# Performance work log

Hardware: AMD Instinct MI355X
Metric: run time of the kernel (lower is better)

The kernel has to match this reference:

```python
import jax, jax.numpy as jnp
import numpy as np

BITS = 16          # number of histogram bins == number of spiking time steps
B, IN_DIM, HID = 16384, 784, 128


def setup_inputs() -> dict:
    key = jax.random.key(0)
    ks = jax.random.split(key, 9)
    dims = [(HID, IN_DIM), (HID, HID), (HID, HID), (IN_DIM, HID)]
    inp = {"features": jax.random.uniform(ks[0], (B, IN_DIM), jnp.float32)}
    for i, (o, d) in enumerate(dims):
        inp["W%d" % i] = jax.random.normal(ks[1 + i], (o, d), jnp.float32) * 0.05
        inp["b%d" % i] = jax.random.normal(ks[5 + i], (o,), jnp.float32) * 0.05
    # np.histogram_bin_edges(bins=16) -> 17 uniformly spaced edges per layer
    in_max = [1.0, 4.0, 4.0, 4.0]
    out_max = [4.0, 4.0, 4.0, 4.0]
    for i in range(4):
        inp["in_bins%d" % i] = jnp.linspace(0.0, in_max[i], BITS + 1, dtype=jnp.float32)
        inp["out_bins%d" % i] = jnp.linspace(0.0, out_max[i], BITS + 1, dtype=jnp.float32)
    return inp


def _spike(t):
    # output[output>1]=1; output[output<1]=0  (==1 stays 1)  -> (t >= 1)
    # totals[output==1] -= 1
    s = (t >= 1.0).astype(t.dtype)
    return s, t - s


def _forward(features, Ws, bs, in_bins, out_bins):
    h_in = [e[1] - e[0] for e in in_bins]    # uniform spike heights
    h_out = [e[1] - e[0] for e in out_bins]
    # set_up_weights: weight *= h_in; weight /= h_out (bias likewise)
    Weff = [Ws[l] * (h_in[l] / h_out[l]) for l in range(4)]
    beff = [bs[l] * (h_in[l] / h_out[l]) for l in range(4)]
    n = features.shape[0]
    # discretize: np.digitize(x, in_bins) - 1, then / 16.0 (non-differentiable)
    act = (jnp.digitize(jax.lax.stop_gradient(features), in_bins[0]) - 1).astype(features.dtype) / BITS
    t_in = jnp.zeros_like(features)                               # input-layer membrane
    totals = tuple(jnp.broadcast_to(beff[l], (n,) + beff[l].shape) for l in range(4))  # reset_totals: totals = bias
    out_acc = jnp.zeros((n, Weff[3].shape[0]), features.dtype)

    def step(carry, _):
        t_in, t0, t1, t2, t3, out = carry
        s_in, t_in = _spike(t_in + act)
        # process_layer: totals += sum(weight * spikes, axis=1) == spikes @ W.T
        s0, t0 = _spike(t0 + s_in @ Weff[0].T)
        s1, t1 = _spike(t1 + s0 @ Weff[1].T)
        s2, t2 = _spike(t2 + s1 @ Weff[2].T)
        s3, t3 = _spike(t3 + s2 @ Weff[3].T)
        return (t_in, t0, t1, t2, t3, out + s3), None

    carry, _ = jax.lax.scan(step, (t_in,) + totals + (out_acc,), None, length=BITS)
    out_spikes = carry[-1]
    # decoder_output_layer.reconstruct: spikes * (out_bins[1] - out_bins[0])
    return out_spikes * h_out[3]


def reference(features, W0, W1, W2, W3, b0, b1, b2, b3,
              in_bins0, in_bins1, in_bins2, in_bins3,
              out_bins0, out_bins1, out_bins2, out_bins3):
    return _forward(features,
                    [W0, W1, W2, W3], [b0, b1, b2, b3],
                    [in_bins0, in_bins1, in_bins2, in_bins3],
                    [out_bins0, out_bins1, out_bins2, out_bins3])
```

## Files before the change

### kernel.cpp

```cpp
#include <hip/hip_runtime.h>

#define IN_DIM 784
#define HID 128
#define NSTEP 16
#define BATCH 16384

constexpr int W0T_OFF = 0;
constexpr int W1T_OFF = W0T_OFF + IN_DIM*HID;
constexpr int W2T_OFF = W1T_OFF + HID*HID;
constexpr int W3T_OFF = W2T_OFF + HID*HID;
constexpr int B0_OFF  = W3T_OFF + HID*IN_DIM;
constexpr int B1_OFF  = B0_OFF + HID;
constexpr int B2_OFF  = B1_OFF + HID;
constexpr int B3_OFF  = B2_OFF + HID;
constexpr int WS_FLOATS = B3_OFF + IN_DIM;

__global__ __launch_bounds__(256) void prep_kernel(
    const float* __restrict__ W0, const float* __restrict__ b0,
    const float* __restrict__ W1, const float* __restrict__ b1,
    const float* __restrict__ W2, const float* __restrict__ b2,
    const float* __restrict__ W3, const float* __restrict__ b3,
    const float* __restrict__ ib0, const float* __restrict__ ob0,
    const float* __restrict__ ib1, const float* __restrict__ ob1,
    const float* __restrict__ ib2, const float* __restrict__ ob2,
    const float* __restrict__ ib3, const float* __restrict__ ob3,
    float* __restrict__ ws)
{
    int idx = blockIdx.x * 256 + threadIdx.x;
    if (idx >= WS_FLOATS) return;
    float r0 = (ib0[1] - ib0[0]) / (ob0[1] - ob0[0]);
    float r1 = (ib1[1] - ib1[0]) / (ob1[1] - ob1[0]);
    float r2 = (ib2[1] - ib2[0]) / (ob2[1] - ob2[0]);
    float r3 = (ib3[1] - ib3[0]) / (ob3[1] - ob3[0]);
    if (idx < W1T_OFF) {
        int t = idx;            int k = t >> 7, j = t & 127;
        ws[idx] = W0[j * IN_DIM + k] * r0;
    } else if (idx < W2T_OFF) {
        int t = idx - W1T_OFF;  int k = t >> 7, j = t & 127;
        ws[idx] = W1[j * HID + k] * r1;
    } else if (idx < W3T_OFF) {
        int t = idx - W2T_OFF;  int k = t >> 7, j = t & 127;
        ws[idx] = W2[j * HID + k] * r2;
    } else if (idx < B0_OFF) {
        int t = idx - W3T_OFF;  int k = t / IN_DIM, o = t % IN_DIM;
        ws[idx] = W3[o * HID + k] * r3;
    } else if (idx < B1_OFF) ws[idx] = b0[idx - B0_OFF] * r0;
    else if (idx < B2_OFF)   ws[idx] = b1[idx - B1_OFF] * r1;
    else if (idx < B3_OFF)   ws[idx] = b2[idx - B2_OFF] * r2;
    else                     ws[idx] = b3[idx - B3_OFF] * r3;
}

__global__ __launch_bounds__(256) void snn_main(
    const float* __restrict__ feat,
    const float* __restrict__ ws,
    const float* __restrict__ ib0,
    const float* __restrict__ ob3,
    float* __restrict__ out)
{
    const int lane = threadIdx.x & 63;
    const int sample = blockIdx.x * 4 + (threadIdx.x >> 6);

    const float* W0t = ws + W0T_OFF;
    const float* W1t = ws + W1T_OFF;
    const float* W2t = ws + W2T_OFF;
    const float* W3t = ws + W3T_OFF;

    float edge[16];
#pragma unroll
    for (int e = 0; e < 16; ++e) edge[e] = ib0[e + 1];

    int m[13];
    {
        const float* frow = feat + (size_t)sample * IN_DIM;
#pragma unroll
        for (int r = 0; r < 13; ++r) {
            int idx = r * 64 + lane;
            int mm = 0;
            if (idx < IN_DIM) {
                float x = frow[idx];
#pragma unroll
                for (int e = 0; e < 16; ++e) mm += (x >= edge[e]) ? 1 : 0;
            }
            m[r] = mm;
        }
    }

    float2 C[16];
#pragma unroll
    for (int mv = 1; mv <= 16; ++mv) {
        float2 ca = make_float2(0.f, 0.f), cb = make_float2(0.f, 0.f);
#pragma unroll
        for (int r = 0; r < 13; ++r) {
            unsigned long long mk = __ballot(m[r] == mv);
            while (mk) {
                int b0 = __builtin_ctzll(mk); mk &= mk - 1;
                float2 w0 = ((const float2*)(W0t + (unsigned)((r << 6) + b0) * HID))[lane];
                if (mk) {
                    int b1 = __builtin_ctzll(mk); mk &= mk - 1;
                    float2 w1 = ((const float2*)(W0t + (unsigned)((r << 6) + b1) * HID))[lane];
                    if (mk) {
                        int b2 = __builtin_ctzll(mk); mk &= mk - 1;
                        float2 w2 = ((const float2*)(W0t + (unsigned)((r << 6) + b2) * HID))[lane];
                        if (mk) {
                            int b3i = __builtin_ctzll(mk); mk &= mk - 1;
                            float2 w3 = ((const float2*)(W0t + (unsigned)((r << 6) + b3i) * HID))[lane];
                            cb.x += w3.x; cb.y += w3.y;
                        }
                        ca.x += w2.x; ca.y += w2.y;
                    }
                    cb.x += w1.x; cb.y += w1.y;
                }
                ca.x += w0.x; ca.y += w0.y;
            }
        }
        C[mv - 1] = make_float2(ca.x + cb.x, ca.y + cb.y);
    }

    float2 t0 = ((const float2*)(ws + B0_OFF))[lane];
    float2 t1 = ((const float2*)(ws + B1_OFF))[lane];
    float2 t2 = ((const float2*)(ws + B2_OFF))[lane];
    float4 t3[4], cnt[4];
    {
        const float4* b3v = (const float4*)(ws + B3_OFF);
#pragma unroll
        for (int r = 0; r < 3; ++r) t3[r] = b3v[r * 64 + lane];
        t3[3] = make_float4(0.f, 0.f, 0.f, 0.f);
        if (lane < 4) t3[3] = b3v[192 + lane];
#pragma unroll
        for (int r = 0; r < 4; ++r) cnt[r] = make_float4(0.f, 0.f, 0.f, 0.f);
    }

    for (int s = 1; s <= NSTEP; ++s) {
#pragma unroll
        for (int mv = 1; mv <= 16; ++mv) {
            if (((s * mv) & 15) < mv) { t0.x += C[mv - 1].x; t0.y += C[mv - 1].y; }
        }
        {
            bool px = (t0.x >= 1.0f), py = (t0.y >= 1.0f);
            unsigned long long mx = __ballot(px);
            unsigned long long my = __ballot(py);
            if (px) t0.x -= 1.0f;
            if (py) t0.y -= 1.0f;
            while (mx) {
                int b = __builtin_ctzll(mx); mx &= mx - 1;
                const float2* col = (const float2*)(W1t + (2 * b) * HID);
                float2 w = col[lane]; t1.x += w.x; t1.y += w.y;
            }
            while (my) {
                int b = __builtin_ctzll(my); my &= my - 1;
                const float2* col = (const float2*)(W1t + (2 * b + 1) * HID);
                float2 w = col[lane]; t1.x += w.x; t1.y += w.y;
            }
        }
        {
            bool px = (t1.x >= 1.0f), py = (t1.y >= 1.0f);
            unsigned long long mx = __ballot(px);
            unsigned long long my = __ballot(py);
            if (px) t1.x -= 1.0f;
            if (py) t1.y -= 1.0f;
            while (mx) {
                int b = __builtin_ctzll(mx); mx &= mx - 1;
                const float2* col = (const float2*)(W2t + (2 * b) * HID);
                float2 w = col[lane]; t2.x += w.x; t2.y += w.y;
            }
            while (my) {
                int b = __builtin_ctzll(my); my &= my - 1;
                const float2* col = (const float2*)(W2t + (2 * b + 1) * HID);
                float2 w = col[lane]; t2.x += w.x; t2.y += w.y;
            }
        }
        {
            bool px = (t2.x >= 1.0f), py = (t2.y >= 1.0f);
            unsigned long long mx = __ballot(px);
            unsigned long long my = __ballot(py);
            if (px) t2.x -= 1.0f;
            if (py) t2.y -= 1.0f;
            while (mx) {
                int b = __builtin_ctzll(mx); mx &= mx - 1;
                const float4* col = (const float4*)(W3t + (2 * b) * IN_DIM);
#pragma unroll
                for (int r = 0; r < 3; ++r) {
                    float4 w = col[r * 64 + lane];
                    t3[r].x += w.x; t3[r].y += w.y; t3[r].z += w.z; t3[r].w += w.w;
                }
                if (lane < 4) {
                    float4 w = col[192 + lane];
                    t3[3].x += w.x; t3[3].y += w.y; t3[3].z += w.z; t3[3].w += w.w;
                }
            }
            while (my) {
                int b = __builtin_ctzll(my); my &= my - 1;
                const float4* col = (const float4*)(W3t + (2 * b + 1) * IN_DIM);
#pragma unroll
                for (int r = 0; r < 3; ++r) {
                    float4 w = col[r * 64 + lane];
                    t3[r].x += w.x; t3[r].y += w.y; t3[r].z += w.z; t3[r].w += w.w;
                }
                if (lane < 4) {
                    float4 w = col[192 + lane];
                    t3[3].x += w.x; t3[3].y += w.y; t3[3].z += w.z; t3[3].w += w.w;
                }
            }
        }
#pragma unroll
        for (int r = 0; r < 4; ++r) {
            if (t3[r].x >= 1.0f) { t3[r].x -= 1.0f; cnt[r].x += 1.0f; }
            if (t3[r].y >= 1.0f) { t3[r].y -= 1.0f; cnt[r].y += 1.0f; }
            if (t3[r].z >= 1.0f) { t3[r].z -= 1.0f; cnt[r].z += 1.0f; }
            if (t3[r].w >= 1.0f) { t3[r].w -= 1.0f; cnt[r].w += 1.0f; }
        }
    }

    const float h = ob3[1] - ob3[0];
    float4* orow = (float4*)(out + (size_t)sample * IN_DIM);
#pragma unroll
    for (int r = 0; r < 3; ++r)
        orow[r * 64 + lane] = make_float4(cnt[r].x * h, cnt[r].y * h, cnt[r].z * h, cnt[r].w * h);
    if (lane < 4)
        orow[192 + lane] = make_float4(cnt[3].x * h, cnt[3].y * h, cnt[3].z * h, cnt[3].w * h);
}

extern "C" void kernel_launch(void* const* d_in, const int* in_sizes, int n_in,
                              void* d_out, int out_size, void* d_ws, size_t ws_size,
                              hipStream_t stream)
{
    const float* feat = (const float*)d_in[0];
    const float* W0  = (const float*)d_in[1];
    const float* b0  = (const float*)d_in[2];
    const float* W1  = (const float*)d_in[3];
    const float* b1  = (const float*)d_in[4];
    const float* W2  = (const float*)d_in[5];
    const float* b2  = (const float*)d_in[6];
    const float* W3  = (const float*)d_in[7];
    const float* b3  = (const float*)d_in[8];
    const float* ib0 = (const float*)d_in[9];
    const float* ob0 = (const float*)d_in[10];
    const float* ib1 = (const float*)d_in[11];
    const float* ob1 = (const float*)d_in[12];
    const float* ib2 = (const float*)d_in[13];
    const float* ob2 = (const float*)d_in[14];
    const float* ib3 = (const float*)d_in[15];
    const float* ob3 = (const float*)d_in[16];
    float* ws  = (float*)d_ws;
    float* op  = (float*)d_out;

    prep_kernel<<<(WS_FLOATS + 255) / 256, 256, 0, stream>>>(
        W0, b0, W1, b1, W2, b2, W3, b3,
        ib0, ob0, ib1, ob1, ib2, ob2, ib3, ob3, ws);

    snn_main<<<BATCH / 4, 256, 0, stream>>>(feat, ws, ib0, ob3, op);
}
```

Before: 466.6 us.

## Stage layer-0 weights through double-buffered LDS chunks shared across block waves

The first-layer precompute now streams W0t in 32-column chunks into a double-buffered shared-memory tile, loaded cooperatively by all 256 threads with a register prefetch of the next chunk. The four waves, one sample each, then read weight columns from LDS instead of each issuing its own global loads. Each chunk's inputs are binned on the fly. This is meant to cut global/L2 traffic for W0 by sharing it across samples in a block. In exchange it adds 32 KB of LDS per block, which may limit occupancy, plus 25 block-wide barriers. The block also loads every W0 column even when no sample uses it.

```diff
diff --git a/kernel.cpp b/kernel.cpp
--- a/kernel.cpp
+++ b/kernel.cpp
@@ -14,6 +14,10 @@
 constexpr int B2_OFF  = B1_OFF + HID;
 constexpr int B3_OFF  = B2_OFF + HID;
 constexpr int WS_FLOATS = B3_OFF + IN_DIM;
+
+constexpr int CHUNK_COLS = 32;
+constexpr int CHUNK_F    = CHUNK_COLS * HID;
+constexpr int NCHUNK     = 25;
 
 __global__ __launch_bounds__(256) void prep_kernel(
     const float* __restrict__ W0, const float* __restrict__ b0,
@@ -57,53 +61,70 @@
     const float* __restrict__ ob3,
     float* __restrict__ out)
 {
-    const int lane = threadIdx.x & 63;
-    const int sample = blockIdx.x * 4 + (threadIdx.x >> 6);
+    __shared__ float smem[2 * CHUNK_F];
+
+    const int tid  = threadIdx.x;
+    const int lane = tid & 63;
+    const int wid  = tid >> 6;
+    const int sample = blockIdx.x * 4 + wid;
 
     const float* W0t = ws + W0T_OFF;
     const float* W1t = ws + W1T_OFF;
     const float* W2t = ws + W2T_OFF;
     const float* W3t = ws + W3T_OFF;
+    const float* frow = feat + (size_t)sample * IN_DIM;
 
     float edge[16];
 #pragma unroll
     for (int e = 0; e < 16; ++e) edge[e] = ib0[e + 1];
 
-    int m[13];
     {
-        const float* frow = feat + (size_t)sample * IN_DIM;
-#pragma unroll
-        for (int r = 0; r < 13; ++r) {
-            int idx = r * 64 + lane;
-            int mm = 0;
-            if (idx < IN_DIM) {
-                float x = frow[idx];
-#pragma unroll
-                for (int e = 0; e < 16; ++e) mm += (x >= edge[e]) ? 1 : 0;
-            }
-            m[r] = mm;
-        }
-    }
+        const float4* g4 = (const float4*)W0t;
+        float4* lb = (float4*)smem;
+#pragma unroll
+        for (int i = 0; i < 4; ++i) lb[i * 256 + tid] = g4[i * 256 + tid];
+    }
+    __syncthreads();
 
     float2 C[16];
 #pragma unroll
-    for (int mv = 1; mv <= 16; ++mv) {
-        float2 ca = make_float2(0.f, 0.f), cb = make_float2(0.f, 0.f);
-#pragma unroll
-        for (int r = 0; r < 13; ++r) {
-            unsigned long long mk = __ballot(m[r] == mv);
+    for (int mv = 0; mv < 16; ++mv) C[mv] = make_float2(0.f, 0.f);
+
+    for (int c = 0; c < NCHUNK; ++c) {
+        float4 rg0, rg1, rg2, rg3;
+        {
+            const float4* g4 = (const float4*)W0t + (size_t)(c + 1) * (CHUNK_F / 4);
+            rg0 = g4[0 * 256 + tid];
+            rg1 = g4[1 * 256 + tid];
+            rg2 = g4[2 * 256 + tid];
+            rg3 = g4[3 * 256 + tid];
+        }
+
+        int col = c * CHUNK_COLS + (lane & 31);
+        bool valid = col < IN_DIM;
+        float x = frow[valid ? col : 0];
+        int mm = 0;
+#pragma unroll
+        for (int e = 0; e < 16; ++e) mm += (x >= edge[e]) ? 1 : 0;
+        if (!valid) mm = -1;
+
+        const float2* bufp = (const float2*)(smem + (c & 1) * CHUNK_F);
+#pragma unroll
+        for (int mv = 1; mv <= 16; ++mv) {
+            unsigned mk = (unsigned)__ballot(mm == mv);
+            float2 ca = make_float2(0.f, 0.f), cb = make_float2(0.f, 0.f);
             while (mk) {
-                int b0 = __builtin_ctzll(mk); mk &= mk - 1;
-                float2 w0 = ((const float2*)(W0t + (unsigned)((r << 6) + b0) * HID))[lane];
+                int b0 = __builtin_ctz(mk); mk &= mk - 1;
+                float2 w0 = bufp[b0 * 64 + lane];
                 if (mk) {
-                    int b1 = __builtin_ctzll(mk); mk &= mk - 1;
-                    float2 w1 = ((const float2*)(W0t + (unsigned)((r << 6) + b1) * HID))[lane];
+                    int b1 = __builtin_ctz(mk); mk &= mk - 1;
+                    float2 w1 = bufp[b1 * 64 + lane];
                     if (mk) {
-                        int b2 = __builtin_ctzll(mk); mk &= mk - 1;
-                        float2 w2 = ((const float2*)(W0t + (unsigned)((r << 6) + b2) * HID))[lane];
+                        int b2 = __builtin_ctz(mk); mk &= mk - 1;
+                        float2 w2 = bufp[b2 * 64 + lane];
                         if (mk) {
-                            int b3i = __builtin_ctzll(mk); mk &= mk - 1;
-                            float2 w3 = ((const float2*)(W0t + (unsigned)((r << 6) + b3i) * HID))[lane];
+                            int b3i = __builtin_ctz(mk); mk &= mk - 1;
+                            float2 w3 = bufp[b3i * 64 + lane];
                             cb.x += w3.x; cb.y += w3.y;
                         }
                         ca.x += w2.x; ca.y += w2.y;
@@ -112,8 +133,18 @@
                 }
                 ca.x += w0.x; ca.y += w0.y;
             }
-        }
-        C[mv - 1] = make_float2(ca.x + cb.x, ca.y + cb.y);
+            C[mv - 1].x += ca.x + cb.x;
+            C[mv - 1].y += ca.y + cb.y;
+        }
+
+        if (c + 1 < NCHUNK) {
+            float4* lb = (float4*)(smem + ((c + 1) & 1) * CHUNK_F);
+            lb[0 * 256 + tid] = rg0;
+            lb[1 * 256 + tid] = rg1;
+            lb[2 * 256 + tid] = rg2;
+            lb[3 * 256 + tid] = rg3;
+        }
+        __syncthreads();
     }
 
     float2 t0 = ((const float2*)(ws + B0_OFF))[lane];
@@ -143,13 +174,13 @@
             if (py) t0.y -= 1.0f;
             while (mx) {
                 int b = __builtin_ctzll(mx); mx &= mx - 1;
-                const float2* col = (const float2*)(W1t + (2 * b) * HID);
-                float2 w = col[lane]; t1.x += w.x; t1.y += w.y;
+                const float2* colp = (const float2*)(W1t + (2 * b) * HID);
+                float2 w = colp[lane]; t1.x += w.x; t1.y += w.y;
             }
             while (my) {
                 int b = __builtin_ctzll(my); my &= my - 1;
-                const float2* col = (const float2*)(W1t + (2 * b + 1) * HID);
-                float2 w = col[lane]; t1.x += w.x; t1.y += w.y;
+                const float2* colp = (const float2*)(W1t + (2 * b + 1) * HID);
+                float2 w = colp[lane]; t1.x += w.x; t1.y += w.y;
             }
         }
         {
@@ -160,13 +191,13 @@
             if (py) t1.y -= 1.0f;
             while (mx) {
                 int b = __builtin_ctzll(mx); mx &= mx - 1;
-                const float2* col = (const float2*)(W2t + (2 * b) * HID);
-                float2 w = col[lane]; t2.x += w.x; t2.y += w.y;
+                const float2* colp = (const float2*)(W2t + (2 * b) * HID);
+                float2 w = colp[lane]; t2.x += w.x; t2.y += w.y;
             }
             while (my) {
                 int b = __builtin_ctzll(my); my &= my - 1;
-                const float2* col = (const float2*)(W2t + (2 * b + 1) * HID);
-                float2 w = col[lane]; t2.x += w.x; t2.y += w.y;
+                const float2* colp = (const float2*)(W2t + (2 * b + 1) * HID);
+                float2 w = colp[lane]; t2.x += w.x; t2.y += w.y;
             }
         }
         {
@@ -177,27 +208,27 @@
             if (py) t2.y -= 1.0f;
             while (mx) {
                 int b = __builtin_ctzll(mx); mx &= mx - 1;
-                const float4* col = (const float4*)(W3t + (2 * b) * IN_DIM);
+                const float4* colp = (const float4*)(W3t + (2 * b) * IN_DIM);
 #pragma unroll
                 for (int r = 0; r < 3; ++r) {
-                    float4 w = col[r * 64 + lane];
+                    float4 w = colp[r * 64 + lane];
                     t3[r].x += w.x; t3[r].y += w.y; t3[r].z += w.z; t3[r].w += w.w;
                 }
                 if (lane < 4) {
-                    float4 w = col[192 + lane];
+                    float4 w = colp[192 + lane];
                     t3[3].x += w.x; t3[3].y += w.y; t3[3].z += w.z; t3[3].w += w.w;
                 }
             }
             while (my) {
                 int b = __builtin_ctzll(my); my &= my - 1;
-                const float4* col = (const float4*)(W3t + (2 * b + 1) * IN_DIM);
+                const float4* colp = (const float4*)(W3t + (2 * b + 1) * IN_DIM);
 #pragma unroll
                 for (int r = 0; r < 3; ++r) {
-                    float4 w = col[r * 64 + lane];
+                    float4 w = colp[r * 64 + lane];
                     t3[r].x += w.x; t3[r].y += w.y; t3[r].z += w.z; t3[r].w += w.w;
                 }
                 if (lane < 4) {
-                    float4 w = col[192 + lane];
+                    float4 w = colp[192 + lane];
                     t3[3].x += w.x; t3[3].y += w.y; t3[3].z += w.z; t3[3].w += w.w;
                 }
             }
```

After: 436.9 us. 1.07x faster.
